# Kernel tuning notes

Hardware: AMD Instinct MI355X
Metric: run time of the kernel (lower is better)

## Reference

```python
import jax, jax.numpy as jnp
import numpy as np


def setup_inputs() -> dict:
    key = jax.random.key(0)
    k1, k2, k3, k4 = jax.random.split(key, 4)
    B, H, S, D = 2, 16, 2048, 64
    q = jax.random.normal(k1, (B, H, S, D), dtype=jnp.float32)
    k = jax.random.normal(k2, (B, H, S, D), dtype=jnp.float32)
    v = jax.random.normal(k3, (B, H, S, D), dtype=jnp.float32)
    mask = jax.random.randint(k4, (1, 1, S, S), 0, 2, dtype=jnp.int32)
    return {"q": q, "k": k, "v": v, "mask": mask}


def reference(q, k, v, mask):
    # scores: [B,H,S,S] -- intentionally materialized as in the original
    d = k.shape[-1]
    scale = 1.0 / jnp.sqrt(jnp.asarray(d, dtype=q.dtype))
    x = jnp.einsum("bhqd,bhkd->bhqk", q, k) * scale
    x = x + mask.astype(x.dtype) * jnp.asarray(-10000.0, dtype=x.dtype)
    p = jax.nn.softmax(x, axis=-1)  # dropout is identity in eval mode
    return jnp.einsum("bhqk,bhkd->bhqd", p, v)
```

## Files before the change

### kernel.cpp

```cpp
#include <hip/hip_runtime.h>


#define S_LEN 2048
#define D_DIM 64
#define N_KT 32
#define LDK 72
#define LDV 72
#define TILE_SHORTS (64 * 72)
#define TILE_BYTES (TILE_SHORTS * 2)
#define NBH 32

typedef __attribute__((ext_vector_type(8))) short bf16x8;
typedef __attribute__((ext_vector_type(16))) float f32x16;
typedef __attribute__((ext_vector_type(2))) __fp16 fp16x2;
typedef unsigned int u32;
typedef unsigned long long u64;

#define C1 0.180336880111121f
#define CM (-14426.9504088896f)

static __device__ __forceinline__ unsigned short f2bf(float f) {
  union { float f; unsigned u; } x; x.f = f;
  return (unsigned short)((x.u + 0x8000u) >> 16);
}
static __device__ __forceinline__ unsigned packbf(float lo, float hi) {
  union { float f; unsigned u; } a, b; a.f = lo; b.f = hi;
  return ((a.u + 0x8000u) >> 16) | ((b.u + 0x8000u) & 0xffff0000u);
}
static __device__ __forceinline__ f32x16 zero16() {
  f32x16 z;
#pragma unroll
  for (int i = 0; i < 16; ++i) z[i] = 0.f;
  return z;
}
static __device__ __forceinline__ void dma16(const u32* g, u32* l) {
  __builtin_amdgcn_global_load_lds(
      (const __attribute__((address_space(1))) u32*)g,
      (__attribute__((address_space(3))) u32*)l, 16, 0, 0);
}
static __device__ __forceinline__ unsigned pkh(float lo, float hi) {
  union { fp16x2 h; unsigned u; } x;
  x.h = __builtin_amdgcn_cvt_pkrtz(lo, hi);
  return x.u;
}

__global__ __launch_bounds__(256) void prep_kv(
    const float* __restrict__ k, const float* __restrict__ v,
    unsigned short* __restrict__ kws, unsigned short* __restrict__ vws) {
  const int kt = blockIdx.x, bh = blockIdx.y;
  const int t = threadIdx.x;
  __shared__ unsigned short Vt[TILE_SHORTS];
  const size_t goff = (size_t)bh * (S_LEN * D_DIM) + (size_t)kt * 64 * D_DIM;
  const float4* kg = (const float4*)(k + goff);
  const float4* vg = (const float4*)(v + goff);
  unsigned short* kimg = kws + (size_t)(bh * N_KT + kt) * TILE_SHORTS;
#pragma unroll
  for (int j = 0; j < 4; ++j) {
    const int i = t + j * 256;
    const int row = i >> 4, c4 = i & 15;
    const float4 x = kg[i];
    ushort4 w;
    w.x = f2bf(x.x); w.y = f2bf(x.y); w.z = f2bf(x.z); w.w = f2bf(x.w);
    *(ushort4*)&kimg[row * LDK + c4 * 4] = w;
    const float4 y = vg[i];
    const int swc = 8 * (((row >> 3) + c4) & 7) + (row & 7);
    const unsigned p01 = pkh(y.x, y.y);
    const unsigned p23 = pkh(y.z, y.w);
    Vt[(4 * c4 + 0) * LDV + swc] = (unsigned short)(p01 & 0xffff);
    Vt[(4 * c4 + 1) * LDV + swc] = (unsigned short)(p01 >> 16);
    Vt[(4 * c4 + 2) * LDV + swc] = (unsigned short)(p23 & 0xffff);
    Vt[(4 * c4 + 3) * LDV + swc] = (unsigned short)(p23 >> 16);
  }
  __syncthreads();
  uint4* vimg = (uint4*)(vws + (size_t)(bh * N_KT + kt) * TILE_SHORTS);
  const uint4* lv = (const uint4*)Vt;
  for (int i = t; i < TILE_BYTES / 16; i += 256) vimg[i] = lv[i];
}

__global__ __launch_bounds__(256) void prep_mask(
    const int* __restrict__ mask, u32* __restrict__ mw) {
  const int wid = blockIdx.x * 4 + (threadIdx.x >> 6);
  const int lane = threadIdx.x & 63;
  const int row = wid >> 5, kt = wid & 31;
  const int mv = mask[(size_t)row * S_LEN + kt * 64 + lane];
  const u64 b = __ballot(mv != 0);
  if (lane < 32) {
    const int hl = lane >> 4, p = lane & 15;
    const int kb = p >> 3, g = (p >> 1) & 3, h = p & 1;
    const int j0 = 32 * kb + 8 * g + 4 * hl + 2 * h;
    u32 w = 0;
    if (!((b >> j0) & 1)) w |= 0x0000FFFFu;
    if (!((b >> (j0 + 1)) & 1)) w |= 0xFFFF0000u;
    mw[((size_t)(row * 2 + hl) * N_KT + kt) * 16 + p] = w;
  }
}

__global__ __launch_bounds__(256, 4) void attn_fwd(
    const float* __restrict__ q, const unsigned short* __restrict__ kws,
    const unsigned short* __restrict__ vws, const u32* __restrict__ mw,
    float* __restrict__ out) {
  const int qt = blockIdx.x;
  const int bh = blockIdx.y;
  const size_t hoff = (size_t)bh * (S_LEN * D_DIM);

  __shared__ unsigned short Ks[2][TILE_SHORTS];
  __shared__ unsigned short Vt[2][TILE_SHORTS];

  const int t = threadIdx.x;
  const int wave = t >> 6;
  const int lane = t & 63;
  const int col = lane & 31;
  const int hl = lane >> 5;
  const int sw = col >> 2;
  const int qh = wave >> 1;
  const int kh = wave & 1;

  const int qg = qt * 64 + qh * 32 + col;

  bf16x8 bQ[4];
  {
    const float* qrow = q + hoff + (size_t)qg * D_DIM;
#pragma unroll
    for (int ks = 0; ks < 4; ++ks) {
      const float4 x0 = *(const float4*)(qrow + ks * 16 + hl * 8);
      const float4 x1 = *(const float4*)(qrow + ks * 16 + hl * 8 + 4);
      union { bf16x8 v; unsigned d[4]; } u;
      u.d[0] = packbf(x0.x * C1, x0.y * C1);
      u.d[1] = packbf(x0.z * C1, x0.w * C1);
      u.d[2] = packbf(x1.x * C1, x1.y * C1);
      u.d[3] = packbf(x1.z * C1, x1.w * C1);
      bQ[ks] = u.v;
    }
  }

  bf16x8 onesA;
  {
    union { bf16x8 v; unsigned d[4]; } u;
    u.d[0] = u.d[1] = u.d[2] = u.d[3] = 0x3C003C00u;
    onesA = u.v;
  }

  const unsigned short* kbase = kws + (size_t)bh * N_KT * TILE_SHORTS;
  const unsigned short* vbase = vws + (size_t)bh * N_KT * TILE_SHORTS;

  f32x16 oT0 = zero16(), oT1 = zero16(), oL = zero16();
  const uint4* mrow = (const uint4*)(mw + (size_t)(qg * 2 + hl) * N_KT * 16);

  {
    const u32* g = (const u32*)(qh == 0 ? kbase : vbase);
    u32* l = qh == 0 ? (u32*)&Ks[0][0] : (u32*)&Vt[0][0];
    if (!kh) {
#pragma unroll
      for (int i = 0; i < 5; ++i) dma16(g + i * 256 + lane * 4, l + i * 256);
    } else {
#pragma unroll
      for (int i = 5; i < 9; ++i) dma16(g + i * 256 + lane * 4, l + i * 256);
    }
  }

  for (int kt = 0; kt < N_KT; ++kt) {
    __syncthreads();
    if (kt + 1 < N_KT) {
      const u32* g = (const u32*)((qh == 0 ? kbase : vbase) +
                                  (size_t)(kt + 1) * TILE_SHORTS);
      u32* l = qh == 0 ? (u32*)&Ks[(kt + 1) & 1][0]
                       : (u32*)&Vt[(kt + 1) & 1][0];
      if (!kh) {
#pragma unroll
        for (int i = 0; i < 5; ++i) dma16(g + i * 256 + lane * 4, l + i * 256);
      } else {
#pragma unroll
        for (int i = 5; i < 9; ++i) dma16(g + i * 256 + lane * 4, l + i * 256);
      }
    }
    const uint4 mq0 = mrow[kt * 4 + kh * 2 + 0];
    const uint4 mq1 = mrow[kt * 4 + kh * 2 + 1];
    const u32 mwv[8] = {mq0.x, mq0.y, mq0.z, mq0.w,
                        mq1.x, mq1.y, mq1.z, mq1.w};
    const unsigned short* Ksb = Ks[kt & 1];
    const unsigned short* Vtb = Vt[kt & 1];

    f32x16 sT = zero16();
#pragma unroll
    for (int ks = 0; ks < 4; ++ks) {
      const bf16x8 aK =
          *(const bf16x8*)&Ksb[(kh * 32 + col) * LDK + ks * 16 + hl * 8];
      sT = __builtin_amdgcn_mfma_f32_32x32x16_bf16(aK, bQ[ks], sT, 0, 0, 0);
    }

    unsigned pw[8];
#pragma unroll
    for (int g2 = 0; g2 < 4; ++g2) {
      const float e0 = __builtin_amdgcn_exp2f(sT[g2 * 4 + 0]);
      const float e1 = __builtin_amdgcn_exp2f(sT[g2 * 4 + 1]);
      const float e2 = __builtin_amdgcn_exp2f(sT[g2 * 4 + 2]);
      const float e3 = __builtin_amdgcn_exp2f(sT[g2 * 4 + 3]);
      pw[g2 * 2 + 0] = pkh(e0, e1) & mwv[g2 * 2 + 0];
      pw[g2 * 2 + 1] = pkh(e2, e3) & mwv[g2 * 2 + 1];
    }

#pragma unroll
    for (int ks2 = 0; ks2 < 2; ++ks2) {
      const unsigned d0 = pw[4 * ks2 + 0], d1 = pw[4 * ks2 + 1];
      const unsigned d2 = pw[4 * ks2 + 2], d3 = pw[4 * ks2 + 3];
      const unsigned s0 = hl ? d0 : d2;
      const unsigned s1 = hl ? d1 : d3;
      const unsigned r0 = (unsigned)__shfl_xor((int)s0, 32);
      const unsigned r1 = (unsigned)__shfl_xor((int)s1, 32);
      union { bf16x8 v; unsigned d[4]; } pf;
      pf.d[0] = hl ? r0 : d0;
      pf.d[1] = hl ? r1 : d1;
      pf.d[2] = hl ? d2 : r0;
      pf.d[3] = hl ? d3 : r1;
      const int cpr = 8 * (((4 * kh + 2 * ks2 + hl) + sw) & 7);
      const bf16x8 aV0 = *(const bf16x8*)&Vtb[col * LDV + cpr];
      const bf16x8 aV1 = *(const bf16x8*)&Vtb[(32 + col) * LDV + cpr];
      oT0 = __builtin_amdgcn_mfma_f32_32x32x16_f16(aV0, pf.v, oT0, 0, 0, 0);
      oT1 = __builtin_amdgcn_mfma_f32_32x32x16_f16(aV1, pf.v, oT1, 0, 0, 0);
      oL = __builtin_amdgcn_mfma_f32_32x32x16_f16(onesA, pf.v, oL, 0, 0, 0);
    }
  }

  __syncthreads();
  {
    float* xb = (float*)&Ks[0][0];
    float* lb = (float*)&Vt[0][0];
    float* xr = xb + (size_t)(qh * 32 + col) * 68;
    if (kh) {
#pragma unroll
      for (int rg = 0; rg < 4; ++rg) {
        float4 w0, w1;
        w0.x = oT0[rg * 4 + 0]; w0.y = oT0[rg * 4 + 1];
        w0.z = oT0[rg * 4 + 2]; w0.w = oT0[rg * 4 + 3];
        w1.x = oT1[rg * 4 + 0]; w1.y = oT1[rg * 4 + 1];
        w1.z = oT1[rg * 4 + 2]; w1.w = oT1[rg * 4 + 3];
        *(float4*)(xr + 8 * rg + 4 * hl) = w0;
        *(float4*)(xr + 32 + 8 * rg + 4 * hl) = w1;
      }
      if (!hl) lb[qh * 32 + col] = oL[0];
    }
    __syncthreads();
    if (!kh) {
      const float inv = 1.0f / (oL[0] + lb[qh * 32 + col]);
      float* orow = out + hoff + (size_t)qg * D_DIM;
#pragma unroll
      for (int rg = 0; rg < 4; ++rg) {
        const float4 a0 = *(const float4*)(xr + 8 * rg + 4 * hl);
        const float4 a1 = *(const float4*)(xr + 32 + 8 * rg + 4 * hl);
        float4 w0, w1;
        w0.x = (oT0[rg * 4 + 0] + a0.x) * inv;
        w0.y = (oT0[rg * 4 + 1] + a0.y) * inv;
        w0.z = (oT0[rg * 4 + 2] + a0.z) * inv;
        w0.w = (oT0[rg * 4 + 3] + a0.w) * inv;
        w1.x = (oT1[rg * 4 + 0] + a1.x) * inv;
        w1.y = (oT1[rg * 4 + 1] + a1.y) * inv;
        w1.z = (oT1[rg * 4 + 2] + a1.z) * inv;
        w1.w = (oT1[rg * 4 + 3] + a1.w) * inv;
        *(float4*)(orow + 8 * rg + 4 * hl) = w0;
        *(float4*)(orow + 32 + 8 * rg + 4 * hl) = w1;
      }
    }
  }
}

__global__ __launch_bounds__(256, 2) void attn_fwd_self(
    const float* __restrict__ q, const float* __restrict__ k,
    const float* __restrict__ v, const int* __restrict__ mask,
    float* __restrict__ out) {
  const int qt = blockIdx.x;
  const int bh = blockIdx.y;
  const size_t hoff = (size_t)bh * (S_LEN * D_DIM);
  __shared__ unsigned short Ks[64 * LDK];
  __shared__ unsigned short Vt[64 * LDV];
  const int t = threadIdx.x;
  const int wave = t >> 6;
  const int lane = t & 63;
  const int col = lane & 31;
  const int hl = lane >> 5;
  const int sw = col >> 2;
  const int qg = qt * 128 + wave * 32 + col;
  bf16x8 bQ[4];
  {
    const float* qrow = q + hoff + (size_t)qg * D_DIM;
#pragma unroll
    for (int ks = 0; ks < 4; ++ks) {
      const float4 x0 = *(const float4*)(qrow + ks * 16 + hl * 8);
      const float4 x1 = *(const float4*)(qrow + ks * 16 + hl * 8 + 4);
      union { bf16x8 v; unsigned d[4]; } u;
      u.d[0] = packbf(x0.x, x0.y);
      u.d[1] = packbf(x0.z, x0.w);
      u.d[2] = packbf(x1.x, x1.y);
      u.d[3] = packbf(x1.z, x1.w);
      bQ[ks] = u.v;
    }
  }
  float4 pk[4], pv[4];
  {
    const float4* kg = (const float4*)(k + hoff);
    const float4* vg = (const float4*)(v + hoff);
#pragma unroll
    for (int j = 0; j < 4; ++j) { pk[j] = kg[t + j * 256]; pv[j] = vg[t + j * 256]; }
  }
  f32x16 oT0 = zero16(), oT1 = zero16();
  float lacc = 0.f;
  const int* mrow = mask + (size_t)qg * S_LEN;
  for (int kt = 0; kt < N_KT; ++kt) {
    __syncthreads();
#pragma unroll
    for (int j = 0; j < 4; ++j) {
      const int i = t + j * 256;
      const int row = i >> 4, c4 = i & 15;
      ushort4 w;
      w.x = f2bf(pk[j].x); w.y = f2bf(pk[j].y);
      w.z = f2bf(pk[j].z); w.w = f2bf(pk[j].w);
      *(ushort4*)&Ks[row * LDK + c4 * 4] = w;
      const int swc = 8 * (((row >> 3) + c4) & 7) + (row & 7);
      Vt[(4 * c4 + 0) * LDV + swc] = f2bf(pv[j].x);
      Vt[(4 * c4 + 1) * LDV + swc] = f2bf(pv[j].y);
      Vt[(4 * c4 + 2) * LDV + swc] = f2bf(pv[j].z);
      Vt[(4 * c4 + 3) * LDV + swc] = f2bf(pv[j].w);
    }
    __syncthreads();
    if (kt + 1 < N_KT) {
      const float4* kg = (const float4*)(k + hoff + (size_t)(kt + 1) * 64 * D_DIM);
      const float4* vg = (const float4*)(v + hoff + (size_t)(kt + 1) * 64 * D_DIM);
#pragma unroll
      for (int j = 0; j < 4; ++j) { pk[j] = kg[t + j * 256]; pv[j] = vg[t + j * 256]; }
    }
    int4 mq[2][4];
#pragma unroll
    for (int kb = 0; kb < 2; ++kb)
#pragma unroll
      for (int g = 0; g < 4; ++g)
        mq[kb][g] = *(const int4*)(mrow + kt * 64 + kb * 32 + g * 8 + hl * 4);
    f32x16 sT0 = zero16(), sT1 = zero16();
#pragma unroll
    for (int ks = 0; ks < 4; ++ks) {
      const bf16x8 aK0 = *(const bf16x8*)&Ks[col * LDK + ks * 16 + hl * 8];
      const bf16x8 aK1 = *(const bf16x8*)&Ks[(32 + col) * LDK + ks * 16 + hl * 8];
      sT0 = __builtin_amdgcn_mfma_f32_32x32x16_bf16(aK0, bQ[ks], sT0, 0, 0, 0);
      sT1 = __builtin_amdgcn_mfma_f32_32x32x16_bf16(aK1, bQ[ks], sT1, 0, 0, 0);
    }
    unsigned pw[2][8];
#pragma unroll
    for (int kb = 0; kb < 2; ++kb) {
      const f32x16 sT = kb ? sT1 : sT0;
      float e[16];
#pragma unroll
      for (int g = 0; g < 4; ++g) {
        const int4 mv = mq[kb][g];
        const int* mvp = &mv.x;
#pragma unroll
        for (int r3 = 0; r3 < 4; ++r3) {
          const int reg = g * 4 + r3;
          const float bias = mvp[r3] ? CM : 0.0f;
          const float ev = __builtin_amdgcn_exp2f(fmaf(sT[reg], C1, bias));
          e[reg] = ev;
          lacc += ev;
        }
        pw[kb][g * 2 + 0] = packbf(e[g * 4 + 0], e[g * 4 + 1]);
        pw[kb][g * 2 + 1] = packbf(e[g * 4 + 2], e[g * 4 + 3]);
      }
    }
#pragma unroll
    for (int ks = 0; ks < 4; ++ks) {
      const int kb = ks >> 1, h = ks & 1;
      const unsigned d0 = pw[kb][4 * h + 0], d1 = pw[kb][4 * h + 1];
      const unsigned d2 = pw[kb][4 * h + 2], d3 = pw[kb][4 * h + 3];
      const unsigned s0 = hl ? d0 : d2;
      const unsigned s1 = hl ? d1 : d3;
      const unsigned r0 = (unsigned)__shfl_xor((int)s0, 32);
      const unsigned r1 = (unsigned)__shfl_xor((int)s1, 32);
      union { bf16x8 v; unsigned d[4]; } pf;
      pf.d[0] = hl ? r0 : d0;
      pf.d[1] = hl ? r1 : d1;
      pf.d[2] = hl ? d2 : r0;
      pf.d[3] = hl ? d3 : r1;
      const int cpr = 8 * (((2 * ks + hl) + sw) & 7);
      const bf16x8 aV0 = *(const bf16x8*)&Vt[col * LDV + cpr];
      const bf16x8 aV1 = *(const bf16x8*)&Vt[(32 + col) * LDV + cpr];
      oT0 = __builtin_amdgcn_mfma_f32_32x32x16_bf16(aV0, pf.v, oT0, 0, 0, 0);
      oT1 = __builtin_amdgcn_mfma_f32_32x32x16_bf16(aV1, pf.v, oT1, 0, 0, 0);
    }
  }
  const float ltot = lacc + __shfl_xor(lacc, 32);
  const float inv = 1.0f / ltot;
  float* orow = out + hoff + (size_t)qg * D_DIM;
#pragma unroll
  for (int rg = 0; rg < 4; ++rg) {
    float4 w0, w1;
    w0.x = oT0[rg * 4 + 0] * inv; w0.y = oT0[rg * 4 + 1] * inv;
    w0.z = oT0[rg * 4 + 2] * inv; w0.w = oT0[rg * 4 + 3] * inv;
    w1.x = oT1[rg * 4 + 0] * inv; w1.y = oT1[rg * 4 + 1] * inv;
    w1.z = oT1[rg * 4 + 2] * inv; w1.w = oT1[rg * 4 + 3] * inv;
    *(float4*)(orow + 8 * rg + 4 * hl) = w0;
    *(float4*)(orow + 32 + 8 * rg + 4 * hl) = w1;
  }
}

extern "C" void kernel_launch(void* const* d_in, const int* in_sizes, int n_in,
                              void* d_out, int out_size, void* d_ws, size_t ws_size,
                              hipStream_t stream) {
  const float* q = (const float*)d_in[0];
  const float* k = (const float*)d_in[1];
  const float* v = (const float*)d_in[2];
  const int* mask = (const int*)d_in[3];
  float* out = (float*)d_out;

  const size_t img_elems = (size_t)NBH * N_KT * TILE_SHORTS;
  const size_t mw_words = (size_t)S_LEN * 2 * N_KT * 16;
  const size_t need = img_elems * 2 * sizeof(unsigned short) + mw_words * 4;

  if (ws_size >= need) {
    unsigned short* kws = (unsigned short*)d_ws;
    unsigned short* vws = kws + img_elems;
    u32* mwp = (u32*)(vws + img_elems);
    prep_kv<<<dim3(N_KT, NBH), dim3(256), 0, stream>>>(k, v, kws, vws);
    prep_mask<<<dim3((S_LEN * N_KT) / 4), dim3(256), 0, stream>>>(mask, mwp);
    attn_fwd<<<dim3(S_LEN / 64, NBH), dim3(256), 0, stream>>>(q, kws, vws, mwp, out);
  } else {
    attn_fwd_self<<<dim3(S_LEN / 128, NBH), dim3(256), 0, stream>>>(q, k, v, mask, out);
  }
}
```

Baseline: 177.9 us.

## Pre-swizzle K/V into MFMA fragment order and load directly from global

The prep kernel now writes K and V tiles already laid out in per-lane MFMA fragment order. The attention kernel loads those fragments straight into registers from global memory, with software double-buffering of K, so the LDS double-buffer, the global-to-LDS DMA and the per-tile barriers go away. The row-sum is taken with fdot2 on the packed probabilities instead of an extra MFMA against a ones matrix, and the mask prep is rewritten to read int4 per thread. The occupancy hint drops from 4 to 3 blocks per CU. The cost is higher register pressure and reliance on L2/global latency hiding without LDS staging.

```diff
diff --git a/kernel.cpp b/kernel.cpp
--- a/kernel.cpp
+++ b/kernel.cpp
@@ -4,11 +4,8 @@
 #define S_LEN 2048
 #define D_DIM 64
 #define N_KT 32
-#define LDK 72
-#define LDV 72
-#define TILE_SHORTS (64 * 72)
-#define TILE_BYTES (TILE_SHORTS * 2)
 #define NBH 32
+#define FRAG_SHORTS 4096
 
 typedef __attribute__((ext_vector_type(8))) short bf16x8;
 typedef __attribute__((ext_vector_type(16))) float f32x16;
@@ -33,11 +30,6 @@
   for (int i = 0; i < 16; ++i) z[i] = 0.f;
   return z;
 }
-static __device__ __forceinline__ void dma16(const u32* g, u32* l) {
-  __builtin_amdgcn_global_load_lds(
-      (const __attribute__((address_space(1))) u32*)g,
-      (__attribute__((address_space(3))) u32*)l, 16, 0, 0);
-}
 static __device__ __forceinline__ unsigned pkh(float lo, float hi) {
   union { fp16x2 h; unsigned u; } x;
   x.h = __builtin_amdgcn_cvt_pkrtz(lo, hi);
@@ -49,11 +41,11 @@
     unsigned short* __restrict__ kws, unsigned short* __restrict__ vws) {
   const int kt = blockIdx.x, bh = blockIdx.y;
   const int t = threadIdx.x;
-  __shared__ unsigned short Vt[TILE_SHORTS];
+  __shared__ unsigned short Kr[64 * 72];
+  __shared__ unsigned short Vr[64 * 72];
   const size_t goff = (size_t)bh * (S_LEN * D_DIM) + (size_t)kt * 64 * D_DIM;
   const float4* kg = (const float4*)(k + goff);
   const float4* vg = (const float4*)(v + goff);
-  unsigned short* kimg = kws + (size_t)(bh * N_KT + kt) * TILE_SHORTS;
 #pragma unroll
   for (int j = 0; j < 4; ++j) {
     const int i = t + j * 256;
@@ -61,41 +53,48 @@
     const float4 x = kg[i];
     ushort4 w;
     w.x = f2bf(x.x); w.y = f2bf(x.y); w.z = f2bf(x.z); w.w = f2bf(x.w);
-    *(ushort4*)&kimg[row * LDK + c4 * 4] = w;
+    *(ushort4*)&Kr[row * 72 + c4 * 4] = w;
     const float4 y = vg[i];
-    const int swc = 8 * (((row >> 3) + c4) & 7) + (row & 7);
-    const unsigned p01 = pkh(y.x, y.y);
-    const unsigned p23 = pkh(y.z, y.w);
-    Vt[(4 * c4 + 0) * LDV + swc] = (unsigned short)(p01 & 0xffff);
-    Vt[(4 * c4 + 1) * LDV + swc] = (unsigned short)(p01 >> 16);
-    Vt[(4 * c4 + 2) * LDV + swc] = (unsigned short)(p23 & 0xffff);
-    Vt[(4 * c4 + 3) * LDV + swc] = (unsigned short)(p23 >> 16);
+    const unsigned p01 = pkh(y.x, y.y), p23 = pkh(y.z, y.w);
+    uint2 vv; vv.x = p01; vv.y = p23;
+    *(uint2*)&Vr[row * 72 + c4 * 4] = vv;
   }
   __syncthreads();
-  uint4* vimg = (uint4*)(vws + (size_t)(bh * N_KT + kt) * TILE_SHORTS);
-  const uint4* lv = (const uint4*)Vt;
-  for (int i = t; i < TILE_BYTES / 16; i += 256) vimg[i] = lv[i];
+  uint4* kimg4 = (uint4*)(kws + (size_t)(bh * N_KT + kt) * FRAG_SHORTS);
+  for (int c = t; c < 512; c += 256) {
+    const int col = c & 31, hlc = (c >> 5) & 1, ks = (c >> 6) & 3, khc = c >> 8;
+    kimg4[c] = *(const uint4*)&Kr[(khc * 32 + col) * 72 + ks * 16 + hlc * 8];
+  }
+  uint4* vimg4 = (uint4*)(vws + (size_t)(bh * N_KT + kt) * FRAG_SHORTS);
+  for (int c = t; c < 512; c += 256) {
+    const int col = c & 31, b = (c >> 5) & 1, hlc = (c >> 6) & 1, kcHi = c >> 7;
+    const int d = b * 32 + col, kk = (2 * kcHi + hlc) * 8;
+    union { unsigned short s[8]; uint4 u; } o;
+#pragma unroll
+    for (int jj = 0; jj < 8; ++jj) o.s[jj] = Vr[(kk + jj) * 72 + d];
+    vimg4[c] = o.u;
+  }
 }
 
 __global__ __launch_bounds__(256) void prep_mask(
     const int* __restrict__ mask, u32* __restrict__ mw) {
-  const int wid = blockIdx.x * 4 + (threadIdx.x >> 6);
-  const int lane = threadIdx.x & 63;
-  const int row = wid >> 5, kt = wid & 31;
-  const int mv = mask[(size_t)row * S_LEN + kt * 64 + lane];
-  const u64 b = __ballot(mv != 0);
-  if (lane < 32) {
-    const int hl = lane >> 4, p = lane & 15;
-    const int kb = p >> 3, g = (p >> 1) & 3, h = p & 1;
-    const int j0 = 32 * kb + 8 * g + 4 * hl + 2 * h;
-    u32 w = 0;
-    if (!((b >> j0) & 1)) w |= 0x0000FFFFu;
-    if (!((b >> (j0 + 1)) & 1)) w |= 0xFFFF0000u;
-    mw[((size_t)(row * 2 + hl) * N_KT + kt) * 16 + p] = w;
-  }
-}
-
-__global__ __launch_bounds__(256, 4) void attn_fwd(
+  const int gt = blockIdx.x * 256 + threadIdx.x;
+  const int row = gt >> 9;
+  const int qi = gt & 511;
+  const int4 m = *(const int4*)(mask + (size_t)row * S_LEN + qi * 4);
+  const int kt = qi >> 4;
+  const int j = (qi << 2) & 63;
+  const int kb = j >> 5, g = (j >> 3) & 3, hl = (j >> 2) & 1;
+  u32 w0 = 0, w1 = 0;
+  if (m.x == 0) w0 |= 0x0000FFFFu;
+  if (m.y == 0) w0 |= 0xFFFF0000u;
+  if (m.z == 0) w1 |= 0x0000FFFFu;
+  if (m.w == 0) w1 |= 0xFFFF0000u;
+  uint2 wv; wv.x = w0; wv.y = w1;
+  *(uint2*)&mw[((size_t)(row * 2 + hl) * N_KT + kt) * 16 + kb * 8 + g * 2] = wv;
+}
+
+__global__ __launch_bounds__(256, 3) void attn_fwd(
     const float* __restrict__ q, const unsigned short* __restrict__ kws,
     const unsigned short* __restrict__ vws, const u32* __restrict__ mw,
     float* __restrict__ out) {
@@ -103,15 +102,11 @@
   const int bh = blockIdx.y;
   const size_t hoff = (size_t)bh * (S_LEN * D_DIM);
 
-  __shared__ unsigned short Ks[2][TILE_SHORTS];
-  __shared__ unsigned short Vt[2][TILE_SHORTS];
-
   const int t = threadIdx.x;
   const int wave = t >> 6;
   const int lane = t & 63;
   const int col = lane & 31;
   const int hl = lane >> 5;
-  const int sw = col >> 2;
   const int qh = wave >> 1;
   const int kh = wave & 1;
 
@@ -133,61 +128,37 @@
     }
   }
 
-  bf16x8 onesA;
-  {
-    union { bf16x8 v; unsigned d[4]; } u;
-    u.d[0] = u.d[1] = u.d[2] = u.d[3] = 0x3C003C00u;
-    onesA = u.v;
-  }
-
-  const unsigned short* kbase = kws + (size_t)bh * N_KT * TILE_SHORTS;
-  const unsigned short* vbase = vws + (size_t)bh * N_KT * TILE_SHORTS;
-
-  f32x16 oT0 = zero16(), oT1 = zero16(), oL = zero16();
+  f32x16 oT0 = zero16(), oT1 = zero16();
+  float lacc = 0.f;
   const uint4* mrow = (const uint4*)(mw + (size_t)(qg * 2 + hl) * N_KT * 16);
 
-  {
-    const u32* g = (const u32*)(qh == 0 ? kbase : vbase);
-    u32* l = qh == 0 ? (u32*)&Ks[0][0] : (u32*)&Vt[0][0];
-    if (!kh) {
-#pragma unroll
-      for (int i = 0; i < 5; ++i) dma16(g + i * 256 + lane * 4, l + i * 256);
-    } else {
-#pragma unroll
-      for (int i = 5; i < 9; ++i) dma16(g + i * 256 + lane * 4, l + i * 256);
-    }
-  }
-
-  for (int kt = 0; kt < N_KT; ++kt) {
-    __syncthreads();
-    if (kt + 1 < N_KT) {
-      const u32* g = (const u32*)((qh == 0 ? kbase : vbase) +
-                                  (size_t)(kt + 1) * TILE_SHORTS);
-      u32* l = qh == 0 ? (u32*)&Ks[(kt + 1) & 1][0]
-                       : (u32*)&Vt[(kt + 1) & 1][0];
-      if (!kh) {
-#pragma unroll
-        for (int i = 0; i < 5; ++i) dma16(g + i * 256 + lane * 4, l + i * 256);
-      } else {
-#pragma unroll
-        for (int i = 5; i < 9; ++i) dma16(g + i * 256 + lane * 4, l + i * 256);
-      }
-    }
+  const unsigned short* kL =
+      kws + (size_t)bh * N_KT * FRAG_SHORTS + kh * 2048 + hl * 256 + col * 8;
+  const unsigned short* vL =
+      vws + (size_t)bh * N_KT * FRAG_SHORTS + kh * 2048 + hl * 512 + col * 8;
+
+#define LDK8(kt_, ks_) (*(const bf16x8*)(kL + (size_t)(kt_) * FRAG_SHORTS + (ks_) * 512))
+#define LDV8(kt_, ks2_, b_) \
+  (*(const bf16x8*)(vL + (size_t)(kt_) * FRAG_SHORTS + (ks2_) * 1024 + (b_) * 256))
+
+#if __has_builtin(__builtin_amdgcn_fdot2)
+  const fp16x2 ones2 = {(__fp16)1.0f, (__fp16)1.0f};
+#endif
+
+  auto body = [&](bf16x8 k0, bf16x8 k1, bf16x8 k2, bf16x8 k3, int kt) {
+    const bf16x8 v00 = LDV8(kt, 0, 0), v01 = LDV8(kt, 0, 1);
+    const bf16x8 v10 = LDV8(kt, 1, 0), v11 = LDV8(kt, 1, 1);
     const uint4 mq0 = mrow[kt * 4 + kh * 2 + 0];
     const uint4 mq1 = mrow[kt * 4 + kh * 2 + 1];
+
+    f32x16 sT = zero16();
+    sT = __builtin_amdgcn_mfma_f32_32x32x16_bf16(k0, bQ[0], sT, 0, 0, 0);
+    sT = __builtin_amdgcn_mfma_f32_32x32x16_bf16(k1, bQ[1], sT, 0, 0, 0);
+    sT = __builtin_amdgcn_mfma_f32_32x32x16_bf16(k2, bQ[2], sT, 0, 0, 0);
+    sT = __builtin_amdgcn_mfma_f32_32x32x16_bf16(k3, bQ[3], sT, 0, 0, 0);
+
     const u32 mwv[8] = {mq0.x, mq0.y, mq0.z, mq0.w,
                         mq1.x, mq1.y, mq1.z, mq1.w};
-    const unsigned short* Ksb = Ks[kt & 1];
-    const unsigned short* Vtb = Vt[kt & 1];
-
-    f32x16 sT = zero16();
-#pragma unroll
-    for (int ks = 0; ks < 4; ++ks) {
-      const bf16x8 aK =
-          *(const bf16x8*)&Ksb[(kh * 32 + col) * LDK + ks * 16 + hl * 8];
-      sT = __builtin_amdgcn_mfma_f32_32x32x16_bf16(aK, bQ[ks], sT, 0, 0, 0);
-    }
-
     unsigned pw[8];
 #pragma unroll
     for (int g2 = 0; g2 < 4; ++g2) {
@@ -195,8 +166,25 @@
       const float e1 = __builtin_amdgcn_exp2f(sT[g2 * 4 + 1]);
       const float e2 = __builtin_amdgcn_exp2f(sT[g2 * 4 + 2]);
       const float e3 = __builtin_amdgcn_exp2f(sT[g2 * 4 + 3]);
-      pw[g2 * 2 + 0] = pkh(e0, e1) & mwv[g2 * 2 + 0];
-      pw[g2 * 2 + 1] = pkh(e2, e3) & mwv[g2 * 2 + 1];
+#if __has_builtin(__builtin_amdgcn_fdot2)
+      const unsigned w0 = pkh(e0, e1) & mwv[g2 * 2 + 0];
+      const unsigned w1 = pkh(e2, e3) & mwv[g2 * 2 + 1];
+      pw[g2 * 2 + 0] = w0;
+      pw[g2 * 2 + 1] = w1;
+      union { unsigned u; fp16x2 h; } c0, c1;
+      c0.u = w0; c1.u = w1;
+      lacc = __builtin_amdgcn_fdot2(c0.h, ones2, lacc, false);
+      lacc = __builtin_amdgcn_fdot2(c1.h, ones2, lacc, false);
+#else
+      const u32 mlo = mwv[g2 * 2 + 0], mhi = mwv[g2 * 2 + 1];
+      const float e0m = (mlo & 0xFFFFu) ? e0 : 0.f;
+      const float e1m = (mlo >> 16) ? e1 : 0.f;
+      const float e2m = (mhi & 0xFFFFu) ? e2 : 0.f;
+      const float e3m = (mhi >> 16) ? e3 : 0.f;
+      pw[g2 * 2 + 0] = pkh(e0m, e1m);
+      pw[g2 * 2 + 1] = pkh(e2m, e3m);
+      lacc += (e0m + e1m) + (e2m + e3m);
+#endif
     }
 
 #pragma unroll
@@ -212,57 +200,70 @@
       pf.d[1] = hl ? r1 : d1;
       pf.d[2] = hl ? d2 : r0;
       pf.d[3] = hl ? d3 : r1;
-      const int cpr = 8 * (((4 * kh + 2 * ks2 + hl) + sw) & 7);
-      const bf16x8 aV0 = *(const bf16x8*)&Vtb[col * LDV + cpr];
-      const bf16x8 aV1 = *(const bf16x8*)&Vtb[(32 + col) * LDV + cpr];
+      const bf16x8 aV0 = ks2 ? v10 : v00;
+      const bf16x8 aV1 = ks2 ? v11 : v01;
       oT0 = __builtin_amdgcn_mfma_f32_32x32x16_f16(aV0, pf.v, oT0, 0, 0, 0);
       oT1 = __builtin_amdgcn_mfma_f32_32x32x16_f16(aV1, pf.v, oT1, 0, 0, 0);
-      oL = __builtin_amdgcn_mfma_f32_32x32x16_f16(onesA, pf.v, oL, 0, 0, 0);
-    }
-  }
-
+    }
+  };
+
+  bf16x8 ka0 = LDK8(0, 0), ka1 = LDK8(0, 1), ka2 = LDK8(0, 2), ka3 = LDK8(0, 3);
+  bf16x8 kb0, kb1, kb2, kb3;
+  for (int kt = 0; kt < N_KT; kt += 2) {
+    kb0 = LDK8(kt + 1, 0); kb1 = LDK8(kt + 1, 1);
+    kb2 = LDK8(kt + 1, 2); kb3 = LDK8(kt + 1, 3);
+    body(ka0, ka1, ka2, ka3, kt);
+    if (kt + 2 < N_KT) {
+      ka0 = LDK8(kt + 2, 0); ka1 = LDK8(kt + 2, 1);
+      ka2 = LDK8(kt + 2, 2); ka3 = LDK8(kt + 2, 3);
+    }
+    body(kb0, kb1, kb2, kb3, kt + 1);
+  }
+#undef LDK8
+#undef LDV8
+
+  __shared__ float xb[64 * 68];
+  __shared__ float lb[64];
+  const float l2 = lacc + __shfl_xor(lacc, 32);
+  float* xr = xb + (size_t)(qh * 32 + col) * 68;
+  if (kh) {
+#pragma unroll
+    for (int rg = 0; rg < 4; ++rg) {
+      float4 w0, w1;
+      w0.x = oT0[rg * 4 + 0]; w0.y = oT0[rg * 4 + 1];
+      w0.z = oT0[rg * 4 + 2]; w0.w = oT0[rg * 4 + 3];
+      w1.x = oT1[rg * 4 + 0]; w1.y = oT1[rg * 4 + 1];
+      w1.z = oT1[rg * 4 + 2]; w1.w = oT1[rg * 4 + 3];
+      *(float4*)(xr + 8 * rg + 4 * hl) = w0;
+      *(float4*)(xr + 32 + 8 * rg + 4 * hl) = w1;
+    }
+    if (!hl) lb[qh * 32 + col] = l2;
+  }
   __syncthreads();
-  {
-    float* xb = (float*)&Ks[0][0];
-    float* lb = (float*)&Vt[0][0];
-    float* xr = xb + (size_t)(qh * 32 + col) * 68;
-    if (kh) {
-#pragma unroll
-      for (int rg = 0; rg < 4; ++rg) {
-        float4 w0, w1;
-        w0.x = oT0[rg * 4 + 0]; w0.y = oT0[rg * 4 + 1];
-        w0.z = oT0[rg * 4 + 2]; w0.w = oT0[rg * 4 + 3];
-        w1.x = oT1[rg * 4 + 0]; w1.y = oT1[rg * 4 + 1];
-        w1.z = oT1[rg * 4 + 2]; w1.w = oT1[rg * 4 + 3];
-        *(float4*)(xr + 8 * rg + 4 * hl) = w0;
-        *(float4*)(xr + 32 + 8 * rg + 4 * hl) = w1;
-      }
-      if (!hl) lb[qh * 32 + col] = oL[0];
-    }
-    __syncthreads();
-    if (!kh) {
-      const float inv = 1.0f / (oL[0] + lb[qh * 32 + col]);
-      float* orow = out + hoff + (size_t)qg * D_DIM;
-#pragma unroll
-      for (int rg = 0; rg < 4; ++rg) {
-        const float4 a0 = *(const float4*)(xr + 8 * rg + 4 * hl);
-        const float4 a1 = *(const float4*)(xr + 32 + 8 * rg + 4 * hl);
-        float4 w0, w1;
-        w0.x = (oT0[rg * 4 + 0] + a0.x) * inv;
-        w0.y = (oT0[rg * 4 + 1] + a0.y) * inv;
-        w0.z = (oT0[rg * 4 + 2] + a0.z) * inv;
-        w0.w = (oT0[rg * 4 + 3] + a0.w) * inv;
-        w1.x = (oT1[rg * 4 + 0] + a1.x) * inv;
-        w1.y = (oT1[rg * 4 + 1] + a1.y) * inv;
-        w1.z = (oT1[rg * 4 + 2] + a1.z) * inv;
-        w1.w = (oT1[rg * 4 + 3] + a1.w) * inv;
-        *(float4*)(orow + 8 * rg + 4 * hl) = w0;
-        *(float4*)(orow + 32 + 8 * rg + 4 * hl) = w1;
-      }
-    }
-  }
-}
-
+  if (!kh) {
+    const float inv = 1.0f / (l2 + lb[qh * 32 + col]);
+    float* orow = out + hoff + (size_t)qg * D_DIM;
+#pragma unroll
+    for (int rg = 0; rg < 4; ++rg) {
+      const float4 a0 = *(const float4*)(xr + 8 * rg + 4 * hl);
+      const float4 a1 = *(const float4*)(xr + 32 + 8 * rg + 4 * hl);
+      float4 w0, w1;
+      w0.x = (oT0[rg * 4 + 0] + a0.x) * inv;
+      w0.y = (oT0[rg * 4 + 1] + a0.y) * inv;
+      w0.z = (oT0[rg * 4 + 2] + a0.z) * inv;
+      w0.w = (oT0[rg * 4 + 3] + a0.w) * inv;
+      w1.x = (oT1[rg * 4 + 0] + a1.x) * inv;
+      w1.y = (oT1[rg * 4 + 1] + a1.y) * inv;
+      w1.z = (oT1[rg * 4 + 2] + a1.z) * inv;
+      w1.w = (oT1[rg * 4 + 3] + a1.w) * inv;
+      *(float4*)(orow + 8 * rg + 4 * hl) = w0;
+      *(float4*)(orow + 32 + 8 * rg + 4 * hl) = w1;
+    }
+  }
+}
+
+#define LDK 72
+#define LDV 72
 __global__ __launch_bounds__(256, 2) void attn_fwd_self(
     const float* __restrict__ q, const float* __restrict__ k,
     const float* __restrict__ v, const int* __restrict__ mask,
@@ -407,16 +408,16 @@
   const int* mask = (const int*)d_in[3];
   float* out = (float*)d_out;
 
-  const size_t img_elems = (size_t)NBH * N_KT * TILE_SHORTS;
+  const size_t img_shorts = (size_t)NBH * N_KT * FRAG_SHORTS;
   const size_t mw_words = (size_t)S_LEN * 2 * N_KT * 16;
-  const size_t need = img_elems * 2 * sizeof(unsigned short) + mw_words * 4;
+  const size_t need = img_shorts * 2 * sizeof(unsigned short) + mw_words * 4;
 
   if (ws_size >= need) {
     unsigned short* kws = (unsigned short*)d_ws;
-    unsigned short* vws = kws + img_elems;
-    u32* mwp = (u32*)(vws + img_elems);
+    unsigned short* vws = kws + img_shorts;
+    u32* mwp = (u32*)(vws + img_shorts);
     prep_kv<<<dim3(N_KT, NBH), dim3(256), 0, stream>>>(k, v, kws, vws);
-    prep_mask<<<dim3((S_LEN * N_KT) / 4), dim3(256), 0, stream>>>(mask, mwp);
+    prep_mask<<<dim3((S_LEN * (S_LEN / 4)) / 256), dim3(256), 0, stream>>>(mask, mwp);
     attn_fwd<<<dim3(S_LEN / 64, NBH), dim3(256), 0, stream>>>(q, kws, vws, mwp, out);
   } else {
     attn_fwd_self<<<dim3(S_LEN / 128, NBH), dim3(256), 0, stream>>>(q, k, v, mask, out);
```

New measurement: 179.9 us. About the same (+1.1%).

## Fuse K/V conversion into attention kernel and remap blocks per XCD

Applied to the files above, without the earlier changes.

Drops the separate prep_kv kernel. The attention kernel now loads fp32 K/V tiles into registers one iteration ahead, converts them to bf16/fp16 and writes the swizzled layout into LDS after the MFMA work, replacing the DMA from pre-converted workspace images. It also rewrites prep_mask to use vectorized int4 loads instead of a ballot, remaps block indices so that each XCD handles a contiguous set of heads for L2 reuse, and adds s_setprio around the MFMA sections. The cost is that every query tile now redundantly converts K/V, which adds VALU work and register pressure, in exchange for removing a kernel launch and the workspace round trip.

```diff
diff --git a/kernel.cpp b/kernel.cpp
--- a/kernel.cpp
+++ b/kernel.cpp
@@ -4,17 +4,15 @@
 #define S_LEN 2048
 #define D_DIM 64
 #define N_KT 32
+#define NBH 32
 #define LDK 72
 #define LDV 72
-#define TILE_SHORTS (64 * 72)
-#define TILE_BYTES (TILE_SHORTS * 2)
-#define NBH 32
+#define K_SHORTS (64 * LDK)
 
 typedef __attribute__((ext_vector_type(8))) short bf16x8;
 typedef __attribute__((ext_vector_type(16))) float f32x16;
 typedef __attribute__((ext_vector_type(2))) __fp16 fp16x2;
 typedef unsigned int u32;
-typedef unsigned long long u64;
 
 #define C1 0.180336880111121f
 #define CM (-14426.9504088896f)
@@ -32,11 +30,6 @@
 #pragma unroll
   for (int i = 0; i < 16; ++i) z[i] = 0.f;
   return z;
-}
-static __device__ __forceinline__ void dma16(const u32* g, u32* l) {
-  __builtin_amdgcn_global_load_lds(
-      (const __attribute__((address_space(1))) u32*)g,
-      (__attribute__((address_space(3))) u32*)l, 16, 0, 0);
 }
 static __device__ __forceinline__ unsigned pkh(float lo, float hi) {
   union { fp16x2 h; unsigned u; } x;
@@ -44,67 +37,38 @@
   return x.u;
 }
 
-__global__ __launch_bounds__(256) void prep_kv(
-    const float* __restrict__ k, const float* __restrict__ v,
-    unsigned short* __restrict__ kws, unsigned short* __restrict__ vws) {
-  const int kt = blockIdx.x, bh = blockIdx.y;
-  const int t = threadIdx.x;
-  __shared__ unsigned short Vt[TILE_SHORTS];
-  const size_t goff = (size_t)bh * (S_LEN * D_DIM) + (size_t)kt * 64 * D_DIM;
-  const float4* kg = (const float4*)(k + goff);
-  const float4* vg = (const float4*)(v + goff);
-  unsigned short* kimg = kws + (size_t)(bh * N_KT + kt) * TILE_SHORTS;
-#pragma unroll
-  for (int j = 0; j < 4; ++j) {
-    const int i = t + j * 256;
-    const int row = i >> 4, c4 = i & 15;
-    const float4 x = kg[i];
-    ushort4 w;
-    w.x = f2bf(x.x); w.y = f2bf(x.y); w.z = f2bf(x.z); w.w = f2bf(x.w);
-    *(ushort4*)&kimg[row * LDK + c4 * 4] = w;
-    const float4 y = vg[i];
-    const int swc = 8 * (((row >> 3) + c4) & 7) + (row & 7);
-    const unsigned p01 = pkh(y.x, y.y);
-    const unsigned p23 = pkh(y.z, y.w);
-    Vt[(4 * c4 + 0) * LDV + swc] = (unsigned short)(p01 & 0xffff);
-    Vt[(4 * c4 + 1) * LDV + swc] = (unsigned short)(p01 >> 16);
-    Vt[(4 * c4 + 2) * LDV + swc] = (unsigned short)(p23 & 0xffff);
-    Vt[(4 * c4 + 3) * LDV + swc] = (unsigned short)(p23 >> 16);
-  }
-  __syncthreads();
-  uint4* vimg = (uint4*)(vws + (size_t)(bh * N_KT + kt) * TILE_SHORTS);
-  const uint4* lv = (const uint4*)Vt;
-  for (int i = t; i < TILE_BYTES / 16; i += 256) vimg[i] = lv[i];
-}
-
 __global__ __launch_bounds__(256) void prep_mask(
     const int* __restrict__ mask, u32* __restrict__ mw) {
-  const int wid = blockIdx.x * 4 + (threadIdx.x >> 6);
-  const int lane = threadIdx.x & 63;
-  const int row = wid >> 5, kt = wid & 31;
-  const int mv = mask[(size_t)row * S_LEN + kt * 64 + lane];
-  const u64 b = __ballot(mv != 0);
-  if (lane < 32) {
-    const int hl = lane >> 4, p = lane & 15;
-    const int kb = p >> 3, g = (p >> 1) & 3, h = p & 1;
-    const int j0 = 32 * kb + 8 * g + 4 * hl + 2 * h;
-    u32 w = 0;
-    if (!((b >> j0) & 1)) w |= 0x0000FFFFu;
-    if (!((b >> (j0 + 1)) & 1)) w |= 0xFFFF0000u;
-    mw[((size_t)(row * 2 + hl) * N_KT + kt) * 16 + p] = w;
-  }
+  const int gt = blockIdx.x * 256 + threadIdx.x;
+  const int q4 = gt & 3;
+  const int kt = (gt >> 2) & 31;
+  const int hl = (gt >> 7) & 1;
+  const int row = gt >> 8;
+  const int j0 = kt * 64 + 32 * (q4 >> 1) + 16 * (q4 & 1) + 4 * hl;
+  const int* mr = mask + (size_t)row * S_LEN;
+  const int4 a = *(const int4*)(mr + j0);
+  const int4 b = *(const int4*)(mr + j0 + 8);
+  uint4 w;
+  w.x = (a.x == 0 ? 0x0000FFFFu : 0u) | (a.y == 0 ? 0xFFFF0000u : 0u);
+  w.y = (a.z == 0 ? 0x0000FFFFu : 0u) | (a.w == 0 ? 0xFFFF0000u : 0u);
+  w.z = (b.x == 0 ? 0x0000FFFFu : 0u) | (b.y == 0 ? 0xFFFF0000u : 0u);
+  w.w = (b.z == 0 ? 0x0000FFFFu : 0u) | (b.w == 0 ? 0xFFFF0000u : 0u);
+  *(uint4*)&mw[((size_t)(row * 2 + hl) * N_KT + kt) * 16 + q4 * 4] = w;
 }
 
 __global__ __launch_bounds__(256, 4) void attn_fwd(
-    const float* __restrict__ q, const unsigned short* __restrict__ kws,
-    const unsigned short* __restrict__ vws, const u32* __restrict__ mw,
+    const float* __restrict__ q, const float* __restrict__ k,
+    const float* __restrict__ v, const u32* __restrict__ mw,
     float* __restrict__ out) {
-  const int qt = blockIdx.x;
-  const int bh = blockIdx.y;
+  const int lin = blockIdx.x + 32 * blockIdx.y;
+  const int xcd = lin & 7;
+  const int wk = lin >> 3;
+  const int qt = wk & 31;
+  const int bh = xcd * 4 + (wk >> 5);
   const size_t hoff = (size_t)bh * (S_LEN * D_DIM);
 
-  __shared__ unsigned short Ks[2][TILE_SHORTS];
-  __shared__ unsigned short Vt[2][TILE_SHORTS];
+  __shared__ unsigned short Ks[2][K_SHORTS];
+  __shared__ unsigned short Vt[2][K_SHORTS];
 
   const int t = threadIdx.x;
   const int wave = t >> 6;
@@ -114,7 +78,6 @@
   const int sw = col >> 2;
   const int qh = wave >> 1;
   const int kh = wave & 1;
-
   const int qg = qt * 64 + qh * 32 + col;
 
   bf16x8 bQ[4];
@@ -140,53 +103,67 @@
     onesA = u.v;
   }
 
-  const unsigned short* kbase = kws + (size_t)bh * N_KT * TILE_SHORTS;
-  const unsigned short* vbase = vws + (size_t)bh * N_KT * TILE_SHORTS;
-
   f32x16 oT0 = zero16(), oT1 = zero16(), oL = zero16();
   const uint4* mrow = (const uint4*)(mw + (size_t)(qg * 2 + hl) * N_KT * 16);
-
-  {
-    const u32* g = (const u32*)(qh == 0 ? kbase : vbase);
-    u32* l = qh == 0 ? (u32*)&Ks[0][0] : (u32*)&Vt[0][0];
-    if (!kh) {
-#pragma unroll
-      for (int i = 0; i < 5; ++i) dma16(g + i * 256 + lane * 4, l + i * 256);
-    } else {
-#pragma unroll
-      for (int i = 5; i < 9; ++i) dma16(g + i * 256 + lane * 4, l + i * 256);
-    }
-  }
+  const float* kbase = k + hoff;
+  const float* vbase = v + hoff;
+
+  auto stage_write = [&](int p, const float4* kx, const float4* vx) {
+#pragma unroll
+    for (int j = 0; j < 4; ++j) {
+      const int i = t + j * 256;
+      const int row = i >> 4, c4 = i & 15;
+      ushort4 w;
+      w.x = f2bf(kx[j].x); w.y = f2bf(kx[j].y);
+      w.z = f2bf(kx[j].z); w.w = f2bf(kx[j].w);
+      *(ushort4*)&Ks[p][row * LDK + c4 * 4] = w;
+      const int swc = 8 * (((row >> 3) + c4) & 7) + (row & 7);
+      const unsigned p01 = pkh(vx[j].x, vx[j].y);
+      const unsigned p23 = pkh(vx[j].z, vx[j].w);
+      Vt[p][(4 * c4 + 0) * LDV + swc] = (unsigned short)(p01 & 0xffff);
+      Vt[p][(4 * c4 + 1) * LDV + swc] = (unsigned short)(p01 >> 16);
+      Vt[p][(4 * c4 + 2) * LDV + swc] = (unsigned short)(p23 & 0xffff);
+      Vt[p][(4 * c4 + 3) * LDV + swc] = (unsigned short)(p23 >> 16);
+    }
+  };
+
+  {
+    const float4* kg = (const float4*)kbase;
+    const float4* vg = (const float4*)vbase;
+    float4 kx[4], vx[4];
+#pragma unroll
+    for (int j = 0; j < 4; ++j) { kx[j] = kg[t + j * 256]; vx[j] = vg[t + j * 256]; }
+    stage_write(0, kx, vx);
+  }
+  __syncthreads();
 
   for (int kt = 0; kt < N_KT; ++kt) {
-    __syncthreads();
+    const int p = kt & 1;
+
+    float4 kx[4], vx[4];
     if (kt + 1 < N_KT) {
-      const u32* g = (const u32*)((qh == 0 ? kbase : vbase) +
-                                  (size_t)(kt + 1) * TILE_SHORTS);
-      u32* l = qh == 0 ? (u32*)&Ks[(kt + 1) & 1][0]
-                       : (u32*)&Vt[(kt + 1) & 1][0];
-      if (!kh) {
-#pragma unroll
-        for (int i = 0; i < 5; ++i) dma16(g + i * 256 + lane * 4, l + i * 256);
-      } else {
-#pragma unroll
-        for (int i = 5; i < 9; ++i) dma16(g + i * 256 + lane * 4, l + i * 256);
-      }
+      const float4* kg = (const float4*)(kbase + (size_t)(kt + 1) * 64 * D_DIM);
+      const float4* vg = (const float4*)(vbase + (size_t)(kt + 1) * 64 * D_DIM);
+#pragma unroll
+      for (int j = 0; j < 4; ++j) { kx[j] = kg[t + j * 256]; vx[j] = vg[t + j * 256]; }
     }
     const uint4 mq0 = mrow[kt * 4 + kh * 2 + 0];
     const uint4 mq1 = mrow[kt * 4 + kh * 2 + 1];
     const u32 mwv[8] = {mq0.x, mq0.y, mq0.z, mq0.w,
                         mq1.x, mq1.y, mq1.z, mq1.w};
-    const unsigned short* Ksb = Ks[kt & 1];
-    const unsigned short* Vtb = Vt[kt & 1];
+
+    const unsigned short* Ksb = Ks[p];
+    const unsigned short* Vtb = Vt[p];
 
     f32x16 sT = zero16();
+    __builtin_amdgcn_s_setprio(1);
 #pragma unroll
     for (int ks = 0; ks < 4; ++ks) {
       const bf16x8 aK =
           *(const bf16x8*)&Ksb[(kh * 32 + col) * LDK + ks * 16 + hl * 8];
       sT = __builtin_amdgcn_mfma_f32_32x32x16_bf16(aK, bQ[ks], sT, 0, 0, 0);
     }
+    __builtin_amdgcn_s_setprio(0);
 
     unsigned pw[8];
 #pragma unroll
@@ -199,6 +176,7 @@
       pw[g2 * 2 + 1] = pkh(e2, e3) & mwv[g2 * 2 + 1];
     }
 
+    __builtin_amdgcn_s_setprio(1);
 #pragma unroll
     for (int ks2 = 0; ks2 < 2; ++ks2) {
       const unsigned d0 = pw[4 * ks2 + 0], d1 = pw[4 * ks2 + 1];
@@ -219,12 +197,16 @@
       oT1 = __builtin_amdgcn_mfma_f32_32x32x16_f16(aV1, pf.v, oT1, 0, 0, 0);
       oL = __builtin_amdgcn_mfma_f32_32x32x16_f16(onesA, pf.v, oL, 0, 0, 0);
     }
-  }
-
-  __syncthreads();
+    __builtin_amdgcn_s_setprio(0);
+
+    if (kt + 1 < N_KT) stage_write(p ^ 1, kx, vx);
+
+    __syncthreads();
+  }
+
   {
     float* xb = (float*)&Ks[0][0];
-    float* lb = (float*)&Vt[0][0];
+    float* lb = (float*)((char*)&Ks[0][0] + 17408);
     float* xr = xb + (size_t)(qh * 32 + col) * 68;
     if (kh) {
 #pragma unroll
@@ -407,17 +389,13 @@
   const int* mask = (const int*)d_in[3];
   float* out = (float*)d_out;
 
-  const size_t img_elems = (size_t)NBH * N_KT * TILE_SHORTS;
   const size_t mw_words = (size_t)S_LEN * 2 * N_KT * 16;
-  const size_t need = img_elems * 2 * sizeof(unsigned short) + mw_words * 4;
+  const size_t need = mw_words * 4;
 
   if (ws_size >= need) {
-    unsigned short* kws = (unsigned short*)d_ws;
-    unsigned short* vws = kws + img_elems;
-    u32* mwp = (u32*)(vws + img_elems);
-    prep_kv<<<dim3(N_KT, NBH), dim3(256), 0, stream>>>(k, v, kws, vws);
-    prep_mask<<<dim3((S_LEN * N_KT) / 4), dim3(256), 0, stream>>>(mask, mwp);
-    attn_fwd<<<dim3(S_LEN / 64, NBH), dim3(256), 0, stream>>>(q, kws, vws, mwp, out);
+    u32* mwp = (u32*)d_ws;
+    prep_mask<<<dim3((S_LEN * 2 * N_KT * 4) / 256), dim3(256), 0, stream>>>(mask, mwp);
+    attn_fwd<<<dim3(S_LEN / 64, NBH), dim3(256), 0, stream>>>(q, k, v, mwp, out);
   } else {
     attn_fwd_self<<<dim3(S_LEN / 128, NBH), dim3(256), 0, stream>>>(q, k, v, mask, out);
   }
```

After: 205.6 us. 1.16x slower.
